# Performance work log

Hardware: AMD Instinct MI355X
Metric: run time of the kernel (lower is better)

Reference implementation:

```python
import jax, jax.numpy as jnp
import numpy as np

C0, C1 = 16, 16              # multiplicities of 0e (scalar) and 1o (vector) irreps
FC_DIM = 32
N_EDGE_FEAT = 32
W_NUMEL = C0*C0 + C1*C0 + C0*C1 + C1*C1   # 1024 tensor-product path weights
D_IN = C0 + 3*C1             # 64


def split_irreps(x):
    # layout: [..., C0 scalars | C1 vectors flattened (C1,3)]
    s = x[..., :C0]
    v = x[..., C0:].reshape(x.shape[:-1] + (C1, 3))
    return s, v


def irrep_linear(s, v, ws, wv):
    # e3nn o3.Linear: per-irrep channel mixing, normalized by sqrt(fan_in)
    s2 = jnp.einsum('...i,io->...o', s, ws) / jnp.sqrt(jnp.float32(ws.shape[0]))
    v2 = jnp.einsum('...ix,io->...ox', v, wv) / jnp.sqrt(jnp.float32(wv.shape[0]))
    return s2, v2


def setup_inputs() -> dict:
    key = jax.random.key(0)
    ks = jax.random.split(key, 12)
    B, N = 2, 256
    node_attr = jax.random.normal(ks[0], (B, N, D_IN), jnp.float32)
    edge_attr = jax.random.normal(ks[1], (B, N, N, N_EDGE_FEAT), jnp.float32)
    edge_sh = jax.random.normal(ks[2], (B, N, N, 4), jnp.float32)  # 1x0e + 1x1o
    mask = jnp.ones((B, N), jnp.float32)
    # learned parameters
    w_lin_in_s = jax.random.normal(ks[3], (C0, C0), jnp.float32)
    w_lin_in_v = jax.random.normal(ks[4], (C1, C1), jnp.float32)
    fc_w1 = jax.random.normal(ks[5], (N_EDGE_FEAT, FC_DIM), jnp.float32) / np.sqrt(N_EDGE_FEAT)
    fc_b1 = jnp.zeros((FC_DIM,), jnp.float32)
    fc_w2 = jax.random.normal(ks[6], (FC_DIM, W_NUMEL), jnp.float32) / np.sqrt(FC_DIM)
    fc_b2 = jnp.zeros((W_NUMEL,), jnp.float32)
    w_lin_out_s = jax.random.normal(ks[7], (C0, C0), jnp.float32)
    w_lin_out_v = jax.random.normal(ks[8], (C1, C1), jnp.float32)
    return dict(node_attr=node_attr, edge_attr=edge_attr, edge_sh=edge_sh, mask=mask,
                w_lin_in_s=w_lin_in_s, w_lin_in_v=w_lin_in_v,
                fc_w1=fc_w1, fc_b1=fc_b1, fc_w2=fc_w2, fc_b2=fc_b2,
                w_lin_out_s=w_lin_out_s, w_lin_out_v=w_lin_out_v)


def tp_conv(node_attr, edge_attr, edge_sh, mask, w_lin_in_s, w_lin_in_v,
            fc_w1, fc_b1, fc_w2, fc_b2, w_lin_out_s, w_lin_out_v):
    B, N, _ = node_attr.shape
    s_na, v_na = split_irreps(node_attr)
    # lin_in
    s_in, v_in = irrep_linear(s_na, v_na, w_lin_in_s, w_lin_in_v)  # [B,N,C0], [B,N,C1,3]
    sh_s = edge_sh[..., 0]      # [B,N,N]
    sh_v = edge_sh[..., 1:4]    # [B,N,N,3]
    # edge MLP producing per-edge tensor-product path weights
    h = jax.nn.relu(edge_attr @ fc_w1 + fc_b1)
    w = h @ fc_w2 + fc_b2       # [B,N,N,W_NUMEL]
    off = 0
    w_ss = w[..., off:off+C0*C0].reshape(B, N, N, C0, C0); off += C0*C0
    w_vv = w[..., off:off+C1*C0].reshape(B, N, N, C1, C0); off += C1*C0
    w_sv = w[..., off:off+C0*C1].reshape(B, N, N, C0, C1); off += C0*C1
    w_vs = w[..., off:off+C1*C1].reshape(B, N, N, C1, C1)
    inv_fan = 1.0 / jnp.sqrt(jnp.float32(C0 + C1))
    # --- FullyConnectedTensorProduct (node i features x edge (i,j) SH) ---
    # 0e output: (0e x 0e -> 0e) + (1o x 1o -> 0e, CG = dot/sqrt(3))
    t_ss = jnp.einsum('bni,bnmio->bnmo', s_in, w_ss) * sh_s[..., None]
    dots = jnp.einsum('bnix,bnmx->bnmi', v_in, sh_v)
    t_vv = jnp.einsum('bnmi,bnmio->bnmo', dots, w_vv) / jnp.sqrt(3.0)
    tp_s = (t_ss + t_vv) * inv_fan                                  # [B,N,N,C0]
    # 1o output: (0e x 1o -> 1o) + (1o x 0e -> 1o)
    t_sv = jnp.einsum('bni,bnmio->bnmo', s_in, w_sv)[..., None] * sh_v[:, :, :, None, :]
    t_vs = jnp.einsum('bnix,bnmio->bnmox', v_in, w_vs) * sh_s[..., None, None]
    tp_v = (t_sv + t_vs) * inv_fan                                  # [B,N,N,C1,3]
    # --- masked reduction over source axis j (dim 2), excluding self ---
    m = mask[:, None, :] * (1.0 - jnp.eye(N, dtype=mask.dtype))[None]  # [B,N,N]
    dsum = jnp.sum(mask, axis=-1) - 1.0                                # [B]
    out_s = jnp.einsum('bnmo,bnm->bno', tp_s, m) / dsum[:, None, None]
    out_v = jnp.einsum('bnmox,bnm->bnox', tp_v, m) / dsum[:, None, None, None]
    # lin_out + residual (out dim == in dim, so F.pad is a no-op)
    out_s, out_v = irrep_linear(out_s, out_v, w_lin_out_s, w_lin_out_v)
    out_s = out_s + s_na
    out_v = out_v + v_na
    return jnp.concatenate([out_s, out_v.reshape(out_v.shape[0], out_v.shape[1], C1*3)], axis=-1)


def reference(node_attr, edge_attr, edge_sh, mask, w_lin_in_s, w_lin_in_v,
              fc_w1, fc_b1, fc_w2, fc_b2, w_lin_out_s, w_lin_out_v):
    return tp_conv(node_attr, edge_attr, edge_sh, mask, w_lin_in_s, w_lin_in_v,
                   fc_w1, fc_b1, fc_w2, fc_b2, w_lin_out_s, w_lin_out_v)
```

## Files before the change

### kernel.cpp

```cpp
#include <hip/hip_runtime.h>
#include <hip/hip_bf16.h>

typedef short short8 __attribute__((ext_vector_type(8)));
typedef float f32x4 __attribute__((ext_vector_type(4)));

__device__ __forceinline__ unsigned short f2bf(float f) {
    union { float f; unsigned int i; } v; v.f = f;
    unsigned int i = v.i;
    unsigned int r = (i + 0x7fffu + ((i >> 16) & 1u)) >> 16;
    return (unsigned short)r;
}

__global__ __launch_bounds__(256, 2)
void tpconv_kernel(const float* __restrict__ node_attr,
                   const float* __restrict__ edge_attr,
                   const float* __restrict__ edge_sh,
                   const float* __restrict__ mask,
                   const float* __restrict__ wlis,
                   const float* __restrict__ wliv,
                   const float* __restrict__ fc_w1,
                   const float* __restrict__ fc_b1,
                   const float* __restrict__ fc_w2,
                   const float* __restrict__ fc_b2,
                   const float* __restrict__ wlos,
                   const float* __restrict__ wlov,
                   float* __restrict__ out)
{
    const int node = blockIdx.x;
    const int b = node >> 8;
    const int n = node & 255;
    const int t = threadIdx.x;

    __shared__ __align__(16) unsigned short s_ea[256 * 32];
    __shared__ __align__(16) unsigned short s_w1t[32 * 32];
    __shared__ __align__(16) float s_wc[4 * 256];
    __shared__ float s_b1[32];
    __shared__ float s_wmask[4];
    __shared__ __align__(16) float s_wp[512];
    __shared__ float s_wp0[16];
    __shared__ __align__(16) float s_mom[128];
    __shared__ float s_mom0[4];
    __shared__ float s_scale;
    __shared__ float s_sin[16];
    __shared__ float s_vin[48];
    __shared__ __align__(16) float s_eff[8 * 256];
    __shared__ float s_pre[16];
    __shared__ float s_prev[48];

    {
        const float4* src = (const float4*)(edge_attr + (size_t)node * (256 * 32));
        #pragma unroll
        for (int it = 0; it < 8; ++it) {
            float4 v = src[it * 256 + t];
            ushort4 u;
            u.x = f2bf(v.x); u.y = f2bf(v.y); u.z = f2bf(v.z); u.w = f2bf(v.w);
            *(ushort4*)&s_ea[(it * 256 + t) * 4] = u;
        }
    }
    {
        float mk = mask[(b << 8) + t];
        float ms = mk;
        ms += __shfl_xor(ms, 1);  ms += __shfl_xor(ms, 2);  ms += __shfl_xor(ms, 4);
        ms += __shfl_xor(ms, 8);  ms += __shfl_xor(ms, 16); ms += __shfl_xor(ms, 32);
        if ((t & 63) == 0) s_wmask[t >> 6] = ms;
        float excl = (t == n) ? 0.0f : mk;
        const float4 sh4 = *(const float4*)(edge_sh + ((size_t)node * 256 + t) * 4);
        s_wc[0 * 256 + t] = excl * sh4.x;
        s_wc[1 * 256 + t] = excl * sh4.y;
        s_wc[2 * 256 + t] = excl * sh4.z;
        s_wc[3 * 256 + t] = excl * sh4.w;
    }
    {
        #pragma unroll
        for (int j = 0; j < 4; ++j) {
            int e = t * 4 + j;
            int f = e >> 5, k = e & 31;
            s_w1t[e] = f2bf(fc_w1[k * 32 + f]);
        }
        if (t < 32) s_b1[t] = fc_b1[t];
    }
    if (t >= 64 && t < 80) {
        int o = t - 64;
        const float* na = node_attr + (size_t)node * 64;
        float a = 0.f;
        #pragma unroll
        for (int i = 0; i < 16; ++i) a += na[i] * wlis[i * 16 + o];
        s_sin[o] = a * 0.25f;
    } else if (t >= 80 && t < 128) {
        int idx = t - 80;
        int o = idx / 3, x = idx - o * 3;
        const float* na = node_attr + (size_t)node * 64;
        float a = 0.f;
        #pragma unroll
        for (int i = 0; i < 16; ++i) a += na[16 + i * 3 + x] * wliv[i * 16 + o];
        s_vin[idx] = a * 0.25f;
    }
    __syncthreads();

    {
        const int wv = t >> 6;
        const int ln = t & 63;
        const int q  = ln >> 4;
        const int fc = ln & 15;
        short8 bf0 = *(const short8*)&s_w1t[fc * 32 + q * 8];
        short8 bf1 = *(const short8*)&s_w1t[(16 + fc) * 32 + q * 8];
        float b1a = s_b1[fc], b1b = s_b1[16 + fc];
        float pmc[4][2] = {{0,0},{0,0},{0,0},{0,0}};
        float pm0[4] = {0,0,0,0};
        #pragma unroll
        for (int tt = 0; tt < 4; ++tt) {
            const int T = wv * 4 + tt;
            short8 af = *(const short8*)&s_ea[(T * 16 + fc) * 32 + q * 8];
            f32x4 z = {0.f, 0.f, 0.f, 0.f};
            f32x4 acc0 = __builtin_amdgcn_mfma_f32_16x16x32_bf16(af, bf0, z, 0, 0, 0);
            f32x4 acc1 = __builtin_amdgcn_mfma_f32_16x16x32_bf16(af, bf1, z, 0, 0, 0);
            f32x4 w0 = *(const f32x4*)&s_wc[0 * 256 + T * 16 + q * 4];
            f32x4 w1 = *(const f32x4*)&s_wc[1 * 256 + T * 16 + q * 4];
            f32x4 w2 = *(const f32x4*)&s_wc[2 * 256 + T * 16 + q * 4];
            f32x4 w3 = *(const f32x4*)&s_wc[3 * 256 + T * 16 + q * 4];
            #pragma unroll
            for (int r = 0; r < 4; ++r) {
                float h0 = acc0[r] + b1a; h0 = h0 > 0.f ? h0 : 0.f;
                float h1 = acc1[r] + b1b; h1 = h1 > 0.f ? h1 : 0.f;
                float wr0 = w0[r], wr1 = w1[r], wr2 = w2[r], wr3 = w3[r];
                pmc[0][0] += h0 * wr0; pmc[0][1] += h1 * wr0;
                pmc[1][0] += h0 * wr1; pmc[1][1] += h1 * wr1;
                pmc[2][0] += h0 * wr2; pmc[2][1] += h1 * wr2;
                pmc[3][0] += h0 * wr3; pmc[3][1] += h1 * wr3;
                pm0[0] += wr0; pm0[1] += wr1; pm0[2] += wr2; pm0[3] += wr3;
            }
        }
        #pragma unroll
        for (int c = 0; c < 4; ++c) {
            #pragma unroll
            for (int ft = 0; ft < 2; ++ft) {
                float v = pmc[c][ft];
                v += __shfl_xor(v, 16);
                v += __shfl_xor(v, 32);
                if (q == 0) s_wp[(wv * 4 + c) * 32 + ft * 16 + fc] = v;
            }
            float v0 = pm0[c];
            v0 += __shfl_xor(v0, 16);
            v0 += __shfl_xor(v0, 32);
            if (ln == 0) s_wp0[wv * 4 + c] = v0;
        }
    }
    __syncthreads();

    if (t < 128) {
        int c = t >> 5, f = t & 31;
        s_mom[c * 32 + f] = s_wp[(0 + c) * 32 + f] + s_wp[(4 + c) * 32 + f]
                          + s_wp[(8 + c) * 32 + f] + s_wp[(12 + c) * 32 + f];
    } else if (t == 128) {
        #pragma unroll
        for (int c = 0; c < 4; ++c)
            s_mom0[c] = s_wp0[c] + s_wp0[4 + c] + s_wp0[8 + c] + s_wp0[12 + c];
    } else if (t == 129) {
        float ds = s_wmask[0] + s_wmask[1] + s_wmask[2] + s_wmask[3] - 1.0f;
        s_scale = 0.17677669529663687f / ds;
    }
    __syncthreads();

    {
        const int e8 = t >> 5;
        const int q8 = t & 31;
        const int col0 = q8 * 8;
        int c, wblk;
        if (e8 == 0)      { c = 0;      wblk = 0; }
        else if (e8 <= 3) { c = e8;     wblk = 1; }
        else if (e8 <= 6) { c = e8 - 3; wblk = 2; }
        else              { c = 0;      wblk = 3; }
        float momf[32];
        #pragma unroll
        for (int f = 0; f < 32; ++f) momf[f] = s_mom[c * 32 + f];
        float m0 = s_mom0[c];
        const float* w2g = fc_w2 + wblk * 256 + col0;
        const float* b2g = fc_b2 + wblk * 256 + col0;
        float acc[8];
        float4 bbA = *(const float4*)b2g;
        float4 bbB = *(const float4*)(b2g + 4);
        acc[0] = m0 * bbA.x; acc[1] = m0 * bbA.y; acc[2] = m0 * bbA.z; acc[3] = m0 * bbA.w;
        acc[4] = m0 * bbB.x; acc[5] = m0 * bbB.y; acc[6] = m0 * bbB.z; acc[7] = m0 * bbB.w;
        #pragma unroll
        for (int f = 0; f < 32; ++f) {
            float4 wA = *(const float4*)(w2g + f * 1024);
            float4 wB = *(const float4*)(w2g + f * 1024 + 4);
            float mf = momf[f];
            acc[0] += mf * wA.x; acc[1] += mf * wA.y; acc[2] += mf * wA.z; acc[3] += mf * wA.w;
            acc[4] += mf * wB.x; acc[5] += mf * wB.y; acc[6] += mf * wB.z; acc[7] += mf * wB.w;
        }
        #pragma unroll
        for (int j = 0; j < 8; ++j) s_eff[e8 * 256 + col0 + j] = acc[j];
    }
    __syncthreads();

    {
        const float inv_s3 = 0.5773502691896258f;
        if (t < 16) {
            int o = t;
            float a = 0.f;
            #pragma unroll
            for (int i = 0; i < 16; ++i) a += s_sin[i] * s_eff[0 * 256 + i * 16 + o];
            float bs = 0.f;
            #pragma unroll
            for (int x = 0; x < 3; ++x)
                #pragma unroll
                for (int i = 0; i < 16; ++i)
                    bs += s_vin[i * 3 + x] * s_eff[(1 + x) * 256 + i * 16 + o];
            s_pre[o] = (a + bs * inv_s3) * s_scale;
        } else if (t < 64) {
            int idx = t - 16;
            int o = idx / 3, x = idx - o * 3;
            float a = 0.f;
            #pragma unroll
            for (int i = 0; i < 16; ++i) a += s_sin[i] * s_eff[(4 + x) * 256 + i * 16 + o];
            float bs = 0.f;
            #pragma unroll
            for (int i = 0; i < 16; ++i) bs += s_vin[i * 3 + x] * s_eff[7 * 256 + i * 16 + o];
            s_prev[idx] = (a + bs) * s_scale;
        }
    }
    __syncthreads();

    if (t < 16) {
        int o = t;
        float a = 0.f;
        #pragma unroll
        for (int i = 0; i < 16; ++i) a += s_pre[i] * wlos[i * 16 + o];
        const float* na = node_attr + (size_t)node * 64;
        out[(size_t)node * 64 + o] = a * 0.25f + na[o];
    } else if (t < 64) {
        int idx = t - 16;
        int o = idx / 3, x = idx - o * 3;
        float a = 0.f;
        #pragma unroll
        for (int i = 0; i < 16; ++i) a += s_prev[i * 3 + x] * wlov[i * 16 + o];
        const float* na = node_attr + (size_t)node * 64;
        out[(size_t)node * 64 + 16 + idx] = a * 0.25f + na[16 + idx];
    }
}

extern "C" void kernel_launch(void* const* d_in, const int* in_sizes, int n_in,
                              void* d_out, int out_size, void* d_ws, size_t ws_size,
                              hipStream_t stream) {
    (void)n_in; (void)d_ws; (void)ws_size; (void)out_size;
    const float* node_attr = (const float*)d_in[0];
    const float* edge_attr = (const float*)d_in[1];
    const float* edge_sh   = (const float*)d_in[2];
    const float* maskp     = (const float*)d_in[3];
    const float* wlis      = (const float*)d_in[4];
    const float* wliv      = (const float*)d_in[5];
    const float* fc_w1     = (const float*)d_in[6];
    const float* fc_b1     = (const float*)d_in[7];
    const float* fc_w2     = (const float*)d_in[8];
    const float* fc_b2     = (const float*)d_in[9];
    const float* wlos      = (const float*)d_in[10];
    const float* wlov      = (const float*)d_in[11];
    float* outp = (float*)d_out;

    int nodes = in_sizes[0] / 64;
    tpconv_kernel<<<dim3(nodes), dim3(256), 0, stream>>>(
        node_attr, edge_attr, edge_sh, maskp, wlis, wliv,
        fc_w1, fc_b1, fc_w2, fc_b2, wlos, wlov, outp);
}
```

Baseline: 95.74 us.

## Load edge features directly into MFMA operands and fuse weight contraction into reduction

Edge features are no longer staged in shared memory. Each lane loads them straight from global memory and packs them to bf16 with a hardware pack-convert instruction before the MFMA, which removes a large LDS buffer and a write/read round trip. The fc_w2 projection and the per-path contraction with the input irreps are merged into one stage per wave group, using cross-lane shuffle reductions instead of materialising the 8x256 effective-weight tile and running a separate serial pass. This cuts LDS use and one barrier phase. In exchange it adds shuffle work and uncoalesced global reads that are 32 bytes per lane inside the MFMA loop.

After: 103.5 us. 8.1% more time.

```diff
diff --git a/kernel.cpp b/kernel.cpp
--- a/kernel.cpp
+++ b/kernel.cpp
@@ -9,6 +9,20 @@
     unsigned int i = v.i;
     unsigned int r = (i + 0x7fffu + ((i >> 16) & 1u)) >> 16;
     return (unsigned short)r;
+}
+
+__device__ __forceinline__ unsigned int cvtpk_bf16(float lo, float hi) {
+    unsigned int r;
+    asm("v_cvt_pk_bf16_f32 %0, %1, %2" : "=v"(r) : "v"(lo), "v"(hi));
+    return r;
+}
+
+__device__ __forceinline__ float xred16(float v) {
+    v += __shfl_xor(v, 4);
+    v += __shfl_xor(v, 8);
+    v += __shfl_xor(v, 16);
+    v += __shfl_xor(v, 32);
+    return v;
 }
 
 __global__ __launch_bounds__(256, 2)
@@ -31,32 +45,20 @@
     const int n = node & 255;
     const int t = threadIdx.x;
 
-    __shared__ __align__(16) unsigned short s_ea[256 * 32];
     __shared__ __align__(16) unsigned short s_w1t[32 * 32];
     __shared__ __align__(16) float s_wc[4 * 256];
     __shared__ float s_b1[32];
     __shared__ float s_wmask[4];
     __shared__ __align__(16) float s_wp[512];
     __shared__ float s_wp0[16];
-    __shared__ __align__(16) float s_mom[128];
+    __shared__ __align__(16) float s_momT[128];
     __shared__ float s_mom0[4];
     __shared__ float s_scale;
     __shared__ float s_sin[16];
     __shared__ float s_vin[48];
-    __shared__ __align__(16) float s_eff[8 * 256];
-    __shared__ float s_pre[16];
-    __shared__ float s_prev[48];
-
-    {
-        const float4* src = (const float4*)(edge_attr + (size_t)node * (256 * 32));
-        #pragma unroll
-        for (int it = 0; it < 8; ++it) {
-            float4 v = src[it * 256 + t];
-            ushort4 u;
-            u.x = f2bf(v.x); u.y = f2bf(v.y); u.z = f2bf(v.z); u.w = f2bf(v.w);
-            *(ushort4*)&s_ea[(it * 256 + t) * 4] = u;
-        }
-    }
+    __shared__ float s_preA[16], s_preB[16];
+    __shared__ float s_prevA[48], s_prevB[48];
+
     {
         float mk = mask[(b << 8) + t];
         float ms = mk;
@@ -72,15 +74,15 @@
     }
     {
         #pragma unroll
-        for (int j = 0; j < 4; ++j) {
-            int e = t * 4 + j;
+        for (int jj = 0; jj < 4; ++jj) {
+            int e = t * 4 + jj;
             int f = e >> 5, k = e & 31;
             s_w1t[e] = f2bf(fc_w1[k * 32 + f]);
         }
         if (t < 32) s_b1[t] = fc_b1[t];
     }
-    if (t >= 64 && t < 80) {
-        int o = t - 64;
+    if (t >= 128 && t < 144) {
+        int o = t - 128;
         const float* na = node_attr + (size_t)node * 64;
         float a = 0.f;
         #pragma unroll
@@ -105,15 +107,22 @@
         short8 bf0 = *(const short8*)&s_w1t[fc * 32 + q * 8];
         short8 bf1 = *(const short8*)&s_w1t[(16 + fc) * 32 + q * 8];
         float b1a = s_b1[fc], b1b = s_b1[16 + fc];
+        const float* ea = edge_attr + (size_t)node * 8192 + fc * 32 + q * 8;
         float pmc[4][2] = {{0,0},{0,0},{0,0},{0,0}};
         float pm0[4] = {0,0,0,0};
         #pragma unroll
         for (int tt = 0; tt < 4; ++tt) {
             const int T = wv * 4 + tt;
-            short8 af = *(const short8*)&s_ea[(T * 16 + fc) * 32 + q * 8];
+            const float4 a0 = *(const float4*)(ea + (size_t)T * 512);
+            const float4 a1 = *(const float4*)(ea + (size_t)T * 512 + 4);
+            union { unsigned int u[4]; short8 s; } cv;
+            cv.u[0] = cvtpk_bf16(a0.x, a0.y);
+            cv.u[1] = cvtpk_bf16(a0.z, a0.w);
+            cv.u[2] = cvtpk_bf16(a1.x, a1.y);
+            cv.u[3] = cvtpk_bf16(a1.z, a1.w);
             f32x4 z = {0.f, 0.f, 0.f, 0.f};
-            f32x4 acc0 = __builtin_amdgcn_mfma_f32_16x16x32_bf16(af, bf0, z, 0, 0, 0);
-            f32x4 acc1 = __builtin_amdgcn_mfma_f32_16x16x32_bf16(af, bf1, z, 0, 0, 0);
+            f32x4 acc0 = __builtin_amdgcn_mfma_f32_16x16x32_bf16(cv.s, bf0, z, 0, 0, 0);
+            f32x4 acc1 = __builtin_amdgcn_mfma_f32_16x16x32_bf16(cv.s, bf1, z, 0, 0, 0);
             f32x4 w0 = *(const f32x4*)&s_wc[0 * 256 + T * 16 + q * 4];
             f32x4 w1 = *(const f32x4*)&s_wc[1 * 256 + T * 16 + q * 4];
             f32x4 w2 = *(const f32x4*)&s_wc[2 * 256 + T * 16 + q * 4];
@@ -149,7 +158,7 @@
 
     if (t < 128) {
         int c = t >> 5, f = t & 31;
-        s_mom[c * 32 + f] = s_wp[(0 + c) * 32 + f] + s_wp[(4 + c) * 32 + f]
+        s_momT[f * 4 + c] = s_wp[(0 + c) * 32 + f] + s_wp[(4 + c) * 32 + f]
                           + s_wp[(8 + c) * 32 + f] + s_wp[(12 + c) * 32 + f];
     } else if (t == 128) {
         #pragma unroll
@@ -162,81 +171,108 @@
     __syncthreads();
 
     {
-        const int e8 = t >> 5;
-        const int q8 = t & 31;
-        const int col0 = q8 * 8;
-        int c, wblk;
-        if (e8 == 0)      { c = 0;      wblk = 0; }
-        else if (e8 <= 3) { c = e8;     wblk = 1; }
-        else if (e8 <= 6) { c = e8 - 3; wblk = 2; }
-        else              { c = 0;      wblk = 3; }
-        float momf[32];
-        #pragma unroll
-        for (int f = 0; f < 32; ++f) momf[f] = s_mom[c * 32 + f];
-        float m0 = s_mom0[c];
-        const float* w2g = fc_w2 + wblk * 256 + col0;
-        const float* b2g = fc_b2 + wblk * 256 + col0;
-        float acc[8];
-        float4 bbA = *(const float4*)b2g;
-        float4 bbB = *(const float4*)(b2g + 4);
-        acc[0] = m0 * bbA.x; acc[1] = m0 * bbA.y; acc[2] = m0 * bbA.z; acc[3] = m0 * bbA.w;
-        acc[4] = m0 * bbB.x; acc[5] = m0 * bbB.y; acc[6] = m0 * bbB.z; acc[7] = m0 * bbB.w;
-        #pragma unroll
-        for (int f = 0; f < 32; ++f) {
-            float4 wA = *(const float4*)(w2g + f * 1024);
-            float4 wB = *(const float4*)(w2g + f * 1024 + 4);
-            float mf = momf[f];
-            acc[0] += mf * wA.x; acc[1] += mf * wA.y; acc[2] += mf * wA.z; acc[3] += mf * wA.w;
-            acc[4] += mf * wB.x; acc[5] += mf * wB.y; acc[6] += mf * wB.z; acc[7] += mf * wB.w;
-        }
-        #pragma unroll
-        for (int j = 0; j < 8; ++j) s_eff[e8 * 256 + col0 + j] = acc[j];
-    }
-    __syncthreads();
-
-    {
-        const float inv_s3 = 0.5773502691896258f;
-        if (t < 16) {
-            int o = t;
-            float a = 0.f;
-            #pragma unroll
-            for (int i = 0; i < 16; ++i) a += s_sin[i] * s_eff[0 * 256 + i * 16 + o];
-            float bs = 0.f;
+        const int g   = t >> 6;
+        const int j   = t & 63;
+        const int i16 = j >> 2;
+        const float* w2g = fc_w2 + g * 256 + j * 4;
+        const f32x4 b2v = *(const f32x4*)(fc_b2 + g * 256 + j * 4);
+        const float si = s_sin[i16];
+        const float vx = s_vin[i16 * 3 + 0], vy = s_vin[i16 * 3 + 1], vz = s_vin[i16 * 3 + 2];
+
+        if (g == 0) {
+            const float m0 = s_mom0[0];
+            f32x4 acc; acc[0] = m0 * b2v[0]; acc[1] = m0 * b2v[1]; acc[2] = m0 * b2v[2]; acc[3] = m0 * b2v[3];
+            #pragma unroll
+            for (int f = 0; f < 32; ++f) {
+                f32x4 wv4 = *(const f32x4*)(w2g + f * 1024);
+                float mv = s_momT[f * 4 + 0];
+                acc[0] += mv * wv4[0]; acc[1] += mv * wv4[1]; acc[2] += mv * wv4[2]; acc[3] += mv * wv4[3];
+            }
+            float p0 = xred16(si * acc[0]), p1 = xred16(si * acc[1]);
+            float p2 = xred16(si * acc[2]), p3 = xred16(si * acc[3]);
+            if (j < 4) { s_preA[j * 4 + 0] = p0; s_preA[j * 4 + 1] = p1;
+                         s_preA[j * 4 + 2] = p2; s_preA[j * 4 + 3] = p3; }
+        } else if (g == 1) {
+            const float cm0 = vx * s_mom0[1] + vy * s_mom0[2] + vz * s_mom0[3];
+            f32x4 acc; acc[0] = cm0 * b2v[0]; acc[1] = cm0 * b2v[1]; acc[2] = cm0 * b2v[2]; acc[3] = cm0 * b2v[3];
+            #pragma unroll
+            for (int f = 0; f < 32; ++f) {
+                f32x4 wv4 = *(const f32x4*)(w2g + f * 1024);
+                f32x4 mv4 = *(const f32x4*)&s_momT[f * 4];
+                float cmf = vx * mv4[1] + vy * mv4[2] + vz * mv4[3];
+                acc[0] += cmf * wv4[0]; acc[1] += cmf * wv4[1]; acc[2] += cmf * wv4[2]; acc[3] += cmf * wv4[3];
+            }
+            float p0 = xred16(acc[0]), p1 = xred16(acc[1]);
+            float p2 = xred16(acc[2]), p3 = xred16(acc[3]);
+            if (j < 4) { s_preB[j * 4 + 0] = p0; s_preB[j * 4 + 1] = p1;
+                         s_preB[j * 4 + 2] = p2; s_preB[j * 4 + 3] = p3; }
+        } else if (g == 2) {
+            float ax[3][4];
+            #pragma unroll
+            for (int x = 0; x < 3; ++x) {
+                float m0x = s_mom0[1 + x];
+                #pragma unroll
+                for (int k = 0; k < 4; ++k) ax[x][k] = m0x * b2v[k];
+            }
+            #pragma unroll
+            for (int f = 0; f < 32; ++f) {
+                f32x4 wv4 = *(const f32x4*)(w2g + f * 1024);
+                f32x4 mv4 = *(const f32x4*)&s_momT[f * 4];
+                #pragma unroll
+                for (int k = 0; k < 4; ++k) {
+                    ax[0][k] += mv4[1] * wv4[k];
+                    ax[1][k] += mv4[2] * wv4[k];
+                    ax[2][k] += mv4[3] * wv4[k];
+                }
+            }
             #pragma unroll
             for (int x = 0; x < 3; ++x)
                 #pragma unroll
-                for (int i = 0; i < 16; ++i)
-                    bs += s_vin[i * 3 + x] * s_eff[(1 + x) * 256 + i * 16 + o];
-            s_pre[o] = (a + bs * inv_s3) * s_scale;
-        } else if (t < 64) {
-            int idx = t - 16;
-            int o = idx / 3, x = idx - o * 3;
-            float a = 0.f;
-            #pragma unroll
-            for (int i = 0; i < 16; ++i) a += s_sin[i] * s_eff[(4 + x) * 256 + i * 16 + o];
-            float bs = 0.f;
-            #pragma unroll
-            for (int i = 0; i < 16; ++i) bs += s_vin[i * 3 + x] * s_eff[7 * 256 + i * 16 + o];
-            s_prev[idx] = (a + bs) * s_scale;
+                for (int k = 0; k < 4; ++k) {
+                    float p = xred16(si * ax[x][k]);
+                    if (j < 4) s_prevA[(j * 4 + k) * 3 + x] = p;
+                }
+        } else {
+            const float m0 = s_mom0[0];
+            f32x4 acc; acc[0] = m0 * b2v[0]; acc[1] = m0 * b2v[1]; acc[2] = m0 * b2v[2]; acc[3] = m0 * b2v[3];
+            #pragma unroll
+            for (int f = 0; f < 32; ++f) {
+                f32x4 wv4 = *(const f32x4*)(w2g + f * 1024);
+                float mv = s_momT[f * 4 + 0];
+                acc[0] += mv * wv4[0]; acc[1] += mv * wv4[1]; acc[2] += mv * wv4[2]; acc[3] += mv * wv4[3];
+            }
+            float vcomp[3] = {vx, vy, vz};
+            #pragma unroll
+            for (int x = 0; x < 3; ++x)
+                #pragma unroll
+                for (int k = 0; k < 4; ++k) {
+                    float p = xred16(vcomp[x] * acc[k]);
+                    if (j < 4) s_prevB[(j * 4 + k) * 3 + x] = p;
+                }
         }
     }
     __syncthreads();
 
     if (t < 16) {
-        int o = t;
+        const float sc = s_scale * 0.25f;
         float a = 0.f;
         #pragma unroll
-        for (int i = 0; i < 16; ++i) a += s_pre[i] * wlos[i * 16 + o];
+        for (int ii = 0; ii < 16; ++ii) {
+            float pre = s_preA[ii] + s_preB[ii] * 0.5773502691896258f;
+            a += pre * wlos[ii * 16 + t];
+        }
         const float* na = node_attr + (size_t)node * 64;
-        out[(size_t)node * 64 + o] = a * 0.25f + na[o];
+        out[(size_t)node * 64 + t] = a * sc + na[t];
     } else if (t < 64) {
         int idx = t - 16;
         int o = idx / 3, x = idx - o * 3;
+        const float sc = s_scale * 0.25f;
         float a = 0.f;
         #pragma unroll
-        for (int i = 0; i < 16; ++i) a += s_prev[i * 3 + x] * wlov[i * 16 + o];
+        for (int ii = 0; ii < 16; ++ii)
+            a += (s_prevA[ii * 3 + x] + s_prevB[ii * 3 + x]) * wlov[ii * 16 + o];
         const float* na = node_attr + (size_t)node * 64;
-        out[(size_t)node * 64 + 16 + idx] = a * 0.25f + na[16 + idx];
+        out[(size_t)node * 64 + 16 + idx] = a * sc + na[16 + idx];
     }
 }
 
```
